# Kernel optimization log

Hardware: AMD Instinct MI355X
Metric: run time of the kernel (lower is better)

Reference implementation:

```python
import jax, jax.numpy as jnp
import numpy as np

BN_EPS = 1e-5


def setup_inputs() -> dict:
    key = jax.random.key(0)
    k1, k2, k3 = jax.random.split(key, 3)
    B, C, H, W = 8, 1024, 48, 48
    Cb = 512
    x = jax.random.normal(k1, (B, C, H, W), dtype=jnp.float32)
    Wg = jax.random.normal(k2, (Cb, C), dtype=jnp.float32) * (1.0 / np.sqrt(C))
    Wz = jax.random.normal(k3, (C, Cb), dtype=jnp.float32) * (1.0 / np.sqrt(Cb))
    gamma = jnp.zeros((C,), dtype=jnp.float32)  # BN weight, const-init 0
    beta = jnp.zeros((C,), dtype=jnp.float32)   # BN bias,  const-init 0
    return {"x": x, "Wg": Wg, "Wz": Wz, "gamma": gamma, "beta": beta}


def reference(x, Wg, Wz, gamma, beta):
    B, C, H, W = x.shape
    HW = H * W
    xf = x.reshape(B, C, HW)                                  # [B,C,N]
    # attn[b,n,m] = <x[b,:,n], x[b,:,m]> / (H*W), softmax over m
    attn = jnp.einsum('bcn,bcm->bnm', xf, xf) / HW            # [B,N,N]
    attn = jax.nn.softmax(attn, axis=-1)
    # g: 1x1 conv C -> Cb (no bias)
    g = jnp.einsum('dc,bcn->bdn', Wg, xf)                     # [B,Cb,N]
    # y[b,d,n] = sum_m attn[b,n,m] * g[b,d,m]
    y = jnp.einsum('bnm,bdm->bdn', attn, g)                   # [B,Cb,N]
    # W_z: 1x1 conv Cb -> C (no bias)
    wy = jnp.einsum('cd,bdn->bcn', Wz, y)                     # [B,C,N]
    # BatchNorm2d in training mode: batch stats over (B, N), biased variance
    mean = jnp.mean(wy, axis=(0, 2), keepdims=True)
    var = jnp.mean(jnp.square(wy - mean), axis=(0, 2), keepdims=True)
    wy_bn = (wy - mean) * jax.lax.rsqrt(var + BN_EPS)
    wy_bn = wy_bn * gamma[None, :, None] + beta[None, :, None]
    z = wy_bn.reshape(B, C, H, W) + x
    return z
```

## Files before the change

kernel.cpp:

```cpp
#include <hip/hip_runtime.h>
#include <hip/hip_bf16.h>
#include <stdint.h>


typedef __bf16 bf16;
typedef __attribute__((ext_vector_type(8))) __bf16 bf16x8;
typedef __attribute__((ext_vector_type(4))) float f32x4;

template <bool F32OUT, bool BNRED>
__global__ __launch_bounds__(256)
void gemm_bt(const bf16* __restrict__ Ag, const bf16* __restrict__ Bg,
             void* __restrict__ Dg, int K, int N,
             long long sA, long long sB, long long sD, float alpha,
             float* __restrict__ ps, float* __restrict__ pq)
{
    __shared__ char lds[32768];
    char* ldsA = lds;
    char* ldsB = lds + 16384;

    const int lane = threadIdx.x & 63;
    const int wv   = threadIdx.x >> 6;
    const int wm   = wv >> 1;
    const int wn   = wv & 1;

    const bf16* Ab = Ag + (long long)blockIdx.z * sA + (long long)blockIdx.y * 128 * K;
    const bf16* Bb = Bg + (long long)blockIdx.z * sB + (long long)blockIdx.x * 128 * K;

    f32x4 acc[4][4];
    #pragma unroll
    for (int i = 0; i < 4; ++i)
        #pragma unroll
        for (int j = 0; j < 4; ++j) {
            f32x4 z = {0.f, 0.f, 0.f, 0.f};
            acc[i][j] = z;
        }

    for (int k0 = 0; k0 < K; k0 += 64) {
        #pragma unroll
        for (int t = 0; t < 4; ++t) {
            int ch  = (wv * 4 + t) * 64 + lane;
            int row = ch >> 3;
            int cc  = (ch & 7) ^ (row & 7);
            bf16x8 va = *(const bf16x8*)(Ab + (long long)row * K + k0 + cc * 8);
            bf16x8 vb = *(const bf16x8*)(Bb + (long long)row * K + k0 + cc * 8);
            *(bf16x8*)(ldsA + ch * 16) = va;
            *(bf16x8*)(ldsB + ch * 16) = vb;
        }
        __syncthreads();

        #pragma unroll
        for (int kk = 0; kk < 64; kk += 32) {
            bf16x8 af[4], bfr[4];
            #pragma unroll
            for (int i = 0; i < 4; ++i) {
                int r = wm * 64 + i * 16 + (lane & 15);
                int c = ((kk >> 3) + (lane >> 4)) ^ (r & 7);
                af[i] = *(const bf16x8*)(ldsA + r * 128 + c * 16);
            }
            #pragma unroll
            for (int j = 0; j < 4; ++j) {
                int r = wn * 64 + j * 16 + (lane & 15);
                int c = ((kk >> 3) + (lane >> 4)) ^ (r & 7);
                bfr[j] = *(const bf16x8*)(ldsB + r * 128 + c * 16);
            }
            #pragma unroll
            for (int i = 0; i < 4; ++i)
                #pragma unroll
                for (int j = 0; j < 4; ++j)
                    acc[i][j] = __builtin_amdgcn_mfma_f32_16x16x32_bf16(af[i], bfr[j], acc[i][j], 0, 0, 0);
        }
        __syncthreads();
    }

    float* bs = (float*)lds;
    float* bq = (float*)(lds + 512);
    if (BNRED) {
        if (threadIdx.x < 128) { bs[threadIdx.x] = 0.f; bq[threadIdx.x] = 0.f; }
        __syncthreads();
    }

    const int m_base = blockIdx.y * 128 + wm * 64;
    const int n_base = blockIdx.x * 128 + wn * 64;
    float s_it[4][4], q_it[4][4];
    #pragma unroll
    for (int i = 0; i < 4; ++i) {
        #pragma unroll
        for (int t = 0; t < 4; ++t) { s_it[i][t] = 0.f; q_it[i][t] = 0.f; }
    }
    #pragma unroll
    for (int i = 0; i < 4; ++i) {
        #pragma unroll
        for (int j = 0; j < 4; ++j) {
            int col = n_base + j * 16 + (lane & 15);
            #pragma unroll
            for (int t = 0; t < 4; ++t) {
                int rowg = m_base + i * 16 + (lane >> 4) * 4 + t;
                float v = acc[i][j][t] * alpha;
                if (F32OUT) ((float*)Dg)[(long long)blockIdx.z * sD + (long long)rowg * N + col] = v;
                else        ((bf16*)Dg)[(long long)blockIdx.z * sD + (long long)rowg * N + col] = (bf16)v;
                if (BNRED) { s_it[i][t] += v; q_it[i][t] += v * v; }
            }
        }
    }

    if (BNRED) {
        #pragma unroll
        for (int i = 0; i < 4; ++i) {
            #pragma unroll
            for (int t = 0; t < 4; ++t) {
                float s = s_it[i][t], q = q_it[i][t];
                #pragma unroll
                for (int m = 1; m < 16; m <<= 1) {
                    s += __shfl_xor(s, m);
                    q += __shfl_xor(q, m);
                }
                if ((lane & 15) == 0) {
                    int cl = wm * 64 + i * 16 + (lane >> 4) * 4 + t;
                    atomicAdd(&bs[cl], s);
                    atomicAdd(&bq[cl], q);
                }
            }
        }
        __syncthreads();
        if (threadIdx.x < 128) {
            int cg = blockIdx.y * 128 + threadIdx.x;
            atomicAdd(&ps[cg], bs[threadIdx.x]);
            atomicAdd(&pq[cg], bq[threadIdx.x]);
        }
    }
}

__global__ __launch_bounds__(256)
void gemm_sym(const bf16* __restrict__ Xg, bf16* __restrict__ Dg,
              int K, int N, long long sX, long long sD, float alpha)
{
    const int NZ = gridDim.z;
    const int d  = blockIdx.z * 171 + blockIdx.x;
    const int zz = d % NZ;
    int tlin     = d / NZ;
    int bi = 0;
    while (tlin >= 18 - bi) { tlin -= 18 - bi; ++bi; }
    const int bj = bi + tlin;
    const bool mir  = (bj > bi);
    const bool diag = (bj == bi);

    __shared__ __align__(16) char lds[35840];
    char* ldsA = lds;
    char* ldsB = diag ? lds : (lds + 16384);

    const int lane = threadIdx.x & 63;
    const int wv   = threadIdx.x >> 6;
    const int wm   = wv >> 1;
    const int wn   = wv & 1;

    const bf16* Ab = Xg + (long long)zz * sX + (long long)bi * 128 * K;
    const bf16* Bb = Xg + (long long)zz * sX + (long long)bj * 128 * K;

    f32x4 acc[4][4];
    #pragma unroll
    for (int i = 0; i < 4; ++i)
        #pragma unroll
        for (int j = 0; j < 4; ++j) {
            f32x4 z = {0.f, 0.f, 0.f, 0.f};
            acc[i][j] = z;
        }

    for (int k0 = 0; k0 < K; k0 += 64) {
        #pragma unroll
        for (int t = 0; t < 4; ++t) {
            int ch  = (wv * 4 + t) * 64 + lane;
            int row = ch >> 3;
            int cc  = (ch & 7) ^ (row & 7);
            bf16x8 va = *(const bf16x8*)(Ab + (long long)row * K + k0 + cc * 8);
            *(bf16x8*)(ldsA + ch * 16) = va;
            if (!diag) {
                bf16x8 vb = *(const bf16x8*)(Bb + (long long)row * K + k0 + cc * 8);
                *(bf16x8*)(ldsB + ch * 16) = vb;
            }
        }
        __syncthreads();

        #pragma unroll
        for (int kk = 0; kk < 64; kk += 32) {
            bf16x8 af[4], bfr[4];
            #pragma unroll
            for (int i = 0; i < 4; ++i) {
                int r = wm * 64 + i * 16 + (lane & 15);
                int c = ((kk >> 3) + (lane >> 4)) ^ (r & 7);
                af[i] = *(const bf16x8*)(ldsA + r * 128 + c * 16);
            }
            #pragma unroll
            for (int j = 0; j < 4; ++j) {
                int r = wn * 64 + j * 16 + (lane & 15);
                int c = ((kk >> 3) + (lane >> 4)) ^ (r & 7);
                bfr[j] = *(const bf16x8*)(ldsB + r * 128 + c * 16);
            }
            #pragma unroll
            for (int i = 0; i < 4; ++i)
                #pragma unroll
                for (int j = 0; j < 4; ++j)
                    acc[i][j] = __builtin_amdgcn_mfma_f32_16x16x32_bf16(af[i], bfr[j], acc[i][j], 0, 0, 0);
        }
        __syncthreads();
    }

    bf16* Db = Dg + (long long)zz * sD;
    bf16 (*tr)[140] = (bf16(*)[140])lds;

    #pragma unroll
    for (int i = 0; i < 4; ++i) {
        #pragma unroll
        for (int j = 0; j < 4; ++j) {
            int c_loc = wn * 64 + j * 16 + (lane & 15);
            int col   = bj * 128 + c_loc;
            #pragma unroll
            for (int t = 0; t < 4; ++t) {
                int r_loc = wm * 64 + i * 16 + (lane >> 4) * 4 + t;
                float v = acc[i][j][t] * alpha;
                Db[(long long)(bi * 128 + r_loc) * N + col] = (bf16)v;
                if (mir) tr[c_loc][r_loc] = (bf16)v;
            }
        }
    }

    if (mir) {
        __syncthreads();
        const int cc = threadIdx.x >> 1, hf = threadIdx.x & 1;
        const bf16* src = &tr[cc][hf * 64];
        bf16* dst = Db + (long long)(bj * 128 + cc) * N + bi * 128 + hf * 64;
        #pragma unroll
        for (int j2 = 0; j2 < 8; ++j2)
            *(bf16x8*)(dst + j2 * 8) = *(const bf16x8*)(src + j2 * 8);
    }
}

__global__ __launch_bounds__(256)
void f32_to_bf16(const float* __restrict__ in, bf16* __restrict__ out, int n)
{
    int idx = (blockIdx.x * 256 + threadIdx.x) * 4;
    if (idx < n) {
        float4 v = *(const float4*)(in + idx);
        out[idx + 0] = (bf16)v.x;
        out[idx + 1] = (bf16)v.y;
        out[idx + 2] = (bf16)v.z;
        out[idx + 3] = (bf16)v.w;
    }
}

__global__ __launch_bounds__(256)
void zero_f32(float* __restrict__ p)
{
    p[blockIdx.x * 256 + threadIdx.x] = 0.f;
}

__global__ __launch_bounds__(256)
void transpose_f32_bf16(const float* __restrict__ x, bf16* __restrict__ xT)
{
    __shared__ bf16 tile[32][33];
    const float* xb = x + (long long)blockIdx.z * 1024 * 2304;
    bf16* xo = xT + (long long)blockIdx.z * 2304 * 1024;
    const int n0 = blockIdx.x * 32;
    const int c0 = blockIdx.y * 32;
    const int tx = threadIdx.x, ty = threadIdx.y;
    #pragma unroll
    for (int i = 0; i < 32; i += 8)
        tile[ty + i][tx] = (bf16)xb[(long long)(c0 + ty + i) * 2304 + n0 + tx];
    __syncthreads();
    #pragma unroll
    for (int i = 0; i < 32; i += 8)
        xo[(long long)(n0 + ty + i) * 1024 + c0 + tx] = tile[tx][ty + i];
}

__global__ __launch_bounds__(256)
void softmax_rows(bf16* __restrict__ S)
{
    bf16* p = S + (long long)blockIdx.x * 2304;
    const int t = threadIdx.x;
    __shared__ float red[256];

    bf16x8 v8 = *(const bf16x8*)(p + t * 8);
    float vt = (float)p[2048 + t];
    float f[8];
    float mx = vt;
    #pragma unroll
    for (int i = 0; i < 8; ++i) { f[i] = (float)v8[i]; mx = fmaxf(mx, f[i]); }

    red[t] = mx; __syncthreads();
    for (int s = 128; s > 0; s >>= 1) { if (t < s) red[t] = fmaxf(red[t], red[t + s]); __syncthreads(); }
    mx = red[0];
    __syncthreads();

    float sum = 0.f;
    #pragma unroll
    for (int i = 0; i < 8; ++i) { f[i] = __expf(f[i] - mx); sum += f[i]; }
    vt = __expf(vt - mx); sum += vt;

    red[t] = sum; __syncthreads();
    for (int s = 128; s > 0; s >>= 1) { if (t < s) red[t] += red[t + s]; __syncthreads(); }
    float inv = 1.0f / red[0];

    bf16x8 o;
    #pragma unroll
    for (int i = 0; i < 8; ++i) o[i] = (bf16)(f[i] * inv);
    *(bf16x8*)(p + t * 8) = o;
    p[2048 + t] = (bf16)(vt * inv);
}

__global__ __launch_bounds__(256)
void bn_finalize(const float* __restrict__ ps, const float* __restrict__ pq,
                 float* __restrict__ mean, float* __restrict__ istd)
{
    int c = blockIdx.x * 256 + threadIdx.x;
    float mu = ps[c] / 18432.0f;
    mean[c] = mu;
    istd[c] = rsqrtf(pq[c] / 18432.0f - mu * mu + 1e-5f);
}

__global__ __launch_bounds__(256)
void bn_apply(const float* __restrict__ wy, const float* __restrict__ x,
              const float* __restrict__ gamma, const float* __restrict__ beta,
              const float* __restrict__ mean, const float* __restrict__ istd,
              float* __restrict__ z)
{
    long long idx = ((long long)blockIdx.x * 256 + threadIdx.x) * 4;
    int c = (int)((idx / 2304) & 1023);
    float sc = gamma[c] * istd[c];
    float sh = beta[c] - mean[c] * sc;
    float4 w  = *(const float4*)(wy + idx);
    float4 xv = *(const float4*)(x + idx);
    float4 o;
    o.x = w.x * sc + sh + xv.x;
    o.y = w.y * sc + sh + xv.y;
    o.z = w.z * sc + sh + xv.z;
    o.w = w.w * sc + sh + xv.w;
    *(float4*)(z + idx) = o;
}

extern "C" void kernel_launch(void* const* d_in, const int* in_sizes, int n_in,
                              void* d_out, int out_size, void* d_ws, size_t ws_size,
                              hipStream_t stream)
{
    const float* x     = (const float*)d_in[0];
    const float* Wg    = (const float*)d_in[1];
    const float* Wz    = (const float*)d_in[2];
    const float* gamma = (const float*)d_in[3];
    const float* beta  = (const float*)d_in[4];
    float* zo = (float*)d_out;

    const int B = 8, C = 1024, Cb = 512, N = 2304;

    const size_t fixedB = ((size_t)Cb * C * 2) * 2 + (size_t)C * 4 * 4 + 4096;
    const size_t perB   = ((size_t)N * C + (size_t)Cb * N + (size_t)N * N + (size_t)N * Cb) * 2 + 1024;
    int BC = 8;
    while (BC > 1 && fixedB + perB * (size_t)BC > ws_size) BC >>= 1;

    char* p = (char*)d_ws;
    auto alloc = [&](size_t bytes) { char* r = p; p += (bytes + 255) & ~(size_t)255; return r; };
    bf16*  Wgb  = (bf16*)alloc((size_t)Cb * C * 2);
    bf16*  Wzb  = (bf16*)alloc((size_t)C * Cb * 2);
    float* psum = (float*)alloc((size_t)C * 4);
    float* pqsm = (float*)alloc((size_t)C * 4);
    float* mean = (float*)alloc((size_t)C * 4);
    float* istd = (float*)alloc((size_t)C * 4);
    bf16*  xT   = (bf16*)alloc((size_t)BC * N * C * 2);
    bf16*  g    = (bf16*)alloc((size_t)BC * Cb * N * 2);
    bf16*  attn = (bf16*)alloc((size_t)BC * N * N * 2);
    bf16*  yT   = (bf16*)alloc((size_t)BC * N * Cb * 2);

    f32_to_bf16<<<dim3((Cb * C) / (256 * 4)), 256, 0, stream>>>(Wg, Wgb, Cb * C);
    f32_to_bf16<<<dim3((C * Cb) / (256 * 4)), 256, 0, stream>>>(Wz, Wzb, C * Cb);
    zero_f32<<<dim3(8), 256, 0, stream>>>(psum);

    for (int cs = 0; cs < B; cs += BC) {
        const float* xc = x + (long long)cs * C * N;
        float* wyc = zo + (long long)cs * C * N;

        transpose_f32_bf16<<<dim3(N / 32, C / 32, BC), dim3(32, 8), 0, stream>>>(xc, xT);

        gemm_bt<false, false><<<dim3(N / 128, Cb / 128, BC), 256, 0, stream>>>(
            Wgb, xT, g, C, N, 0, (long long)N * C, (long long)Cb * N, 1.0f, nullptr, nullptr);

        gemm_sym<<<dim3(171, 1, BC), 256, 0, stream>>>(
            xT, attn, C, N, (long long)N * C, (long long)N * N, 1.0f / 2304.0f);

        softmax_rows<<<dim3(BC * N), 256, 0, stream>>>(attn);

        gemm_bt<false, false><<<dim3(Cb / 128, N / 128, BC), 256, 0, stream>>>(
            attn, g, yT, N, Cb, (long long)N * N, (long long)Cb * N, (long long)N * Cb, 1.0f,
            nullptr, nullptr);

        gemm_bt<true, true><<<dim3(N / 128, C / 128, BC), 256, 0, stream>>>(
            Wzb, yT, wyc, Cb, N, 0, (long long)N * Cb, (long long)C * N, 1.0f, psum, pqsm);
    }

    bn_finalize<<<dim3(C / 256), 256, 0, stream>>>(psum, pqsm, mean, istd);
    bn_apply<<<dim3((B * C * N) / (256 * 4)), 256, 0, stream>>>(zo, x, gamma, beta, mean, istd, zo);
}
```

Baseline: 418.1 us.

## Store pre-BN output as bf16, remap GEMM grids batch-innermost, vectorize transpose LDS writes

```diff
diff --git a/kernel.cpp b/kernel.cpp
--- a/kernel.cpp
+++ b/kernel.cpp
@@ -5,15 +5,24 @@
 
 typedef __bf16 bf16;
 typedef __attribute__((ext_vector_type(8))) __bf16 bf16x8;
+typedef __attribute__((ext_vector_type(4))) __bf16 bf16x4;
 typedef __attribute__((ext_vector_type(4))) float f32x4;
 
-template <bool F32OUT, bool BNRED>
-__global__ __launch_bounds__(256)
-void gemm_bt(const bf16* __restrict__ Ag, const bf16* __restrict__ Bg,
-             void* __restrict__ Dg, int K, int N,
-             long long sA, long long sB, long long sD, float alpha,
-             float* __restrict__ ps, float* __restrict__ pq)
-{
+template <bool F32OUT, bool BNRED, bool BXI>
+__global__ __launch_bounds__(256)
+void gemm_btz(const bf16* __restrict__ Ag, const bf16* __restrict__ Bg,
+              void* __restrict__ Dg, int K, int N,
+              long long sA, long long sB, long long sD, float alpha,
+              float* __restrict__ ps, float* __restrict__ pq, int nInner, int nz)
+{
+    const int d  = blockIdx.x;
+    const int zz = d % nz;
+    const int t0 = d / nz;
+    const int bI = t0 % nInner;
+    const int bO = t0 / nInner;
+    const int bx = BXI ? bI : bO;
+    const int by = BXI ? bO : bI;
+
     __shared__ char lds[32768];
     char* ldsA = lds;
     char* ldsB = lds + 16384;
@@ -23,8 +32,8 @@
     const int wm   = wv >> 1;
     const int wn   = wv & 1;
 
-    const bf16* Ab = Ag + (long long)blockIdx.z * sA + (long long)blockIdx.y * 128 * K;
-    const bf16* Bb = Bg + (long long)blockIdx.z * sB + (long long)blockIdx.x * 128 * K;
+    const bf16* Ab = Ag + (long long)zz * sA + (long long)by * 128 * K;
+    const bf16* Bb = Bg + (long long)zz * sB + (long long)bx * 128 * K;
 
     f32x4 acc[4][4];
     #pragma unroll
@@ -79,8 +88,8 @@
         __syncthreads();
     }
 
-    const int m_base = blockIdx.y * 128 + wm * 64;
-    const int n_base = blockIdx.x * 128 + wn * 64;
+    const int m_base = by * 128 + wm * 64;
+    const int n_base = bx * 128 + wn * 64;
     float s_it[4][4], q_it[4][4];
     #pragma unroll
     for (int i = 0; i < 4; ++i) {
@@ -96,8 +105,8 @@
             for (int t = 0; t < 4; ++t) {
                 int rowg = m_base + i * 16 + (lane >> 4) * 4 + t;
                 float v = acc[i][j][t] * alpha;
-                if (F32OUT) ((float*)Dg)[(long long)blockIdx.z * sD + (long long)rowg * N + col] = v;
-                else        ((bf16*)Dg)[(long long)blockIdx.z * sD + (long long)rowg * N + col] = (bf16)v;
+                if (F32OUT) ((float*)Dg)[(long long)zz * sD + (long long)rowg * N + col] = v;
+                else        ((bf16*)Dg)[(long long)zz * sD + (long long)rowg * N + col] = (bf16)v;
                 if (BNRED) { s_it[i][t] += v; q_it[i][t] += v * v; }
             }
         }
@@ -123,7 +132,7 @@
         }
         __syncthreads();
         if (threadIdx.x < 128) {
-            int cg = blockIdx.y * 128 + threadIdx.x;
+            int cg = by * 128 + threadIdx.x;
             atomicAdd(&ps[cg], bs[threadIdx.x]);
             atomicAdd(&pq[cg], bq[threadIdx.x]);
         }
@@ -213,12 +222,17 @@
         for (int j = 0; j < 4; ++j) {
             int c_loc = wn * 64 + j * 16 + (lane & 15);
             int col   = bj * 128 + c_loc;
+            bf16x4 tv;
             #pragma unroll
             for (int t = 0; t < 4; ++t) {
                 int r_loc = wm * 64 + i * 16 + (lane >> 4) * 4 + t;
                 float v = acc[i][j][t] * alpha;
                 Db[(long long)(bi * 128 + r_loc) * N + col] = (bf16)v;
-                if (mir) tr[c_loc][r_loc] = (bf16)v;
+                tv[t] = (bf16)v;
+            }
+            if (mir) {
+                int r_base = wm * 64 + i * 16 + (lane >> 4) * 4;
+                *(bf16x4*)(&tr[c_loc][r_base]) = tv;
             }
         }
     }
@@ -317,23 +331,29 @@
 }
 
 __global__ __launch_bounds__(256)
-void bn_apply(const float* __restrict__ wy, const float* __restrict__ x,
-              const float* __restrict__ gamma, const float* __restrict__ beta,
-              const float* __restrict__ mean, const float* __restrict__ istd,
-              float* __restrict__ z)
-{
-    long long idx = ((long long)blockIdx.x * 256 + threadIdx.x) * 4;
+void bn_apply_b(const bf16* __restrict__ wy, const float* __restrict__ x,
+                const float* __restrict__ gamma, const float* __restrict__ beta,
+                const float* __restrict__ mean, const float* __restrict__ istd,
+                float* __restrict__ z)
+{
+    long long idx = ((long long)blockIdx.x * 256 + threadIdx.x) * 8;
     int c = (int)((idx / 2304) & 1023);
     float sc = gamma[c] * istd[c];
     float sh = beta[c] - mean[c] * sc;
-    float4 w  = *(const float4*)(wy + idx);
-    float4 xv = *(const float4*)(x + idx);
-    float4 o;
-    o.x = w.x * sc + sh + xv.x;
-    o.y = w.y * sc + sh + xv.y;
-    o.z = w.z * sc + sh + xv.z;
-    o.w = w.w * sc + sh + xv.w;
-    *(float4*)(z + idx) = o;
+    bf16x8 w  = *(const bf16x8*)(wy + idx);
+    float4 x0 = *(const float4*)(x + idx);
+    float4 x1 = *(const float4*)(x + idx + 4);
+    float4 o0, o1;
+    o0.x = (float)w[0] * sc + sh + x0.x;
+    o0.y = (float)w[1] * sc + sh + x0.y;
+    o0.z = (float)w[2] * sc + sh + x0.z;
+    o0.w = (float)w[3] * sc + sh + x0.w;
+    o1.x = (float)w[4] * sc + sh + x1.x;
+    o1.y = (float)w[5] * sc + sh + x1.y;
+    o1.z = (float)w[6] * sc + sh + x1.z;
+    o1.w = (float)w[7] * sc + sh + x1.w;
+    *(float4*)(z + idx)     = o0;
+    *(float4*)(z + idx + 4) = o1;
 }
 
 extern "C" void kernel_launch(void* const* d_in, const int* in_sizes, int n_in,
@@ -350,7 +370,8 @@
     const int B = 8, C = 1024, Cb = 512, N = 2304;
 
     const size_t fixedB = ((size_t)Cb * C * 2) * 2 + (size_t)C * 4 * 4 + 4096;
-    const size_t perB   = ((size_t)N * C + (size_t)Cb * N + (size_t)N * N + (size_t)N * Cb) * 2 + 1024;
+    const size_t perB   = ((size_t)N * C + (size_t)Cb * N + (size_t)N * N + (size_t)N * Cb
+                           + (size_t)C * N) * 2 + 1280;
     int BC = 8;
     while (BC > 1 && fixedB + perB * (size_t)BC > ws_size) BC >>= 1;
 
@@ -366,6 +387,7 @@
     bf16*  g    = (bf16*)alloc((size_t)BC * Cb * N * 2);
     bf16*  attn = (bf16*)alloc((size_t)BC * N * N * 2);
     bf16*  yT   = (bf16*)alloc((size_t)BC * N * Cb * 2);
+    bf16*  wyb  = (bf16*)alloc((size_t)BC * C * N * 2);
 
     f32_to_bf16<<<dim3((Cb * C) / (256 * 4)), 256, 0, stream>>>(Wg, Wgb, Cb * C);
     f32_to_bf16<<<dim3((C * Cb) / (256 * 4)), 256, 0, stream>>>(Wz, Wzb, C * Cb);
@@ -373,26 +395,52 @@
 
     for (int cs = 0; cs < B; cs += BC) {
         const float* xc = x + (long long)cs * C * N;
-        float* wyc = zo + (long long)cs * C * N;
 
         transpose_f32_bf16<<<dim3(N / 32, C / 32, BC), dim3(32, 8), 0, stream>>>(xc, xT);
 
-        gemm_bt<false, false><<<dim3(N / 128, Cb / 128, BC), 256, 0, stream>>>(
-            Wgb, xT, g, C, N, 0, (long long)N * C, (long long)Cb * N, 1.0f, nullptr, nullptr);
+        gemm_btz<false, false, false><<<dim3(18 * 4 * BC), 256, 0, stream>>>(
+            Wgb, xT, g, C, N, 0, (long long)N * C, (long long)Cb * N, 1.0f,
+            nullptr, nullptr, 4, BC);
 
         gemm_sym<<<dim3(171, 1, BC), 256, 0, stream>>>(
             xT, attn, C, N, (long long)N * C, (long long)N * N, 1.0f / 2304.0f);
 
         softmax_rows<<<dim3(BC * N), 256, 0, stream>>>(attn);
 
-        gemm_bt<false, false><<<dim3(Cb / 128, N / 128, BC), 256, 0, stream>>>(
+        gemm_btz<false, false, true><<<dim3(4 * 18 * BC), 256, 0, stream>>>(
             attn, g, yT, N, Cb, (long long)N * N, (long long)Cb * N, (long long)N * Cb, 1.0f,
-            nullptr, nullptr);
-
-        gemm_bt<true, true><<<dim3(N / 128, C / 128, BC), 256, 0, stream>>>(
-            Wzb, yT, wyc, Cb, N, 0, (long long)N * Cb, (long long)C * N, 1.0f, psum, pqsm);
+            nullptr, nullptr, 4, BC);
+
+        gemm_btz<false, true, false><<<dim3(18 * 8 * BC), 256, 0, stream>>>(
+            Wzb, yT, wyb + (long long)0, Cb, N, 0, (long long)N * Cb, (long long)C * N, 1.0f,
+            psum, pqsm, 8, BC);
+
     }
 
     bn_finalize<<<dim3(C / 256), 256, 0, stream>>>(psum, pqsm, mean, istd);
-    bn_apply<<<dim3((B * C * N) / (256 * 4)), 256, 0, stream>>>(zo, x, gamma, beta, mean, istd, zo);
-}
+
+    if (BC == B) {
+        bn_apply_b<<<dim3((B * C * N) / (256 * 8)), 256, 0, stream>>>(
+            wyb, x, gamma, beta, mean, istd, zo);
+    } else {
+        for (int cs = 0; cs < B; cs += BC) {
+            const float* xc = x + (long long)cs * C * N;
+            float* zoc = zo + (long long)cs * C * N;
+            transpose_f32_bf16<<<dim3(N / 32, C / 32, BC), dim3(32, 8), 0, stream>>>(xc, xT);
+            gemm_btz<false, false, false><<<dim3(18 * 4 * BC), 256, 0, stream>>>(
+                Wgb, xT, g, C, N, 0, (long long)N * C, (long long)Cb * N, 1.0f,
+                nullptr, nullptr, 4, BC);
+            gemm_sym<<<dim3(171, 1, BC), 256, 0, stream>>>(
+                xT, attn, C, N, (long long)N * C, (long long)N * N, 1.0f / 2304.0f);
+            softmax_rows<<<dim3(BC * N), 256, 0, stream>>>(attn);
+            gemm_btz<false, false, true><<<dim3(4 * 18 * BC), 256, 0, stream>>>(
+                attn, g, yT, N, Cb, (long long)N * N, (long long)Cb * N, (long long)N * Cb,
+                1.0f, nullptr, nullptr, 4, BC);
+            gemm_btz<false, false, false><<<dim3(18 * 8 * BC), 256, 0, stream>>>(
+                Wzb, yT, wyb, Cb, N, 0, (long long)N * Cb, (long long)C * N, 1.0f,
+                nullptr, nullptr, 8, BC);
+            bn_apply_b<<<dim3((BC * C * N) / (256 * 8)), 256, 0, stream>>>(
+                wyb, xc, gamma, beta, mean, istd, zoc);
+        }
+    }
+}
```

Result: faster. 404.9 us (-3.2%).
